# Kernel tuning notes

Measured on AMD Instinct MI355X. Metric: run time of the kernel, lower is better.

The kernel has to match this reference:

```python
import jax, jax.numpy as jnp
import numpy as np

DICT = 32768
TOP_K = 128
LN_EPS = 1e-5


def setup_inputs() -> dict:
    key = jax.random.key(0)
    k_x, k_we, k_be, k_wd, k_bd = jax.random.split(key, 5)
    B, S, D = 4, 2048, 768
    x = jax.random.normal(k_x, (B, S, D), dtype=jnp.float32)
    # nn.Linear stores weight as [out, in]; init scaled roughly like orthogonal gains
    W_enc = jax.random.normal(k_we, (DICT, D), dtype=jnp.float32) / np.sqrt(D)
    b_enc = jax.random.normal(k_be, (DICT,), dtype=jnp.float32) * 0.01
    W_dec = jax.random.normal(k_wd, (D, DICT), dtype=jnp.float32) * (0.1 / np.sqrt(DICT))
    b_dec = jax.random.normal(k_bd, (D,), dtype=jnp.float32) * 0.01
    ln_gamma = jnp.ones((DICT,), dtype=jnp.float32)
    ln_beta = jnp.zeros((DICT,), dtype=jnp.float32)
    return {"x": x, "W_enc": W_enc, "b_enc": b_enc, "ln_gamma": ln_gamma,
            "ln_beta": ln_beta, "W_dec": W_dec, "b_dec": b_dec}


def _layernorm(z, gamma, beta):
    mu = jnp.mean(z, axis=-1, keepdims=True)
    var = jnp.mean(jnp.square(z - mu), axis=-1, keepdims=True)
    return (z - mu) * jax.lax.rsqrt(var + LN_EPS) * gamma + beta


def _top_k_activation(z, k):
    # keep top-k values per row, zero elsewhere (scatter, like torch.scatter_)
    vals, idx = jax.lax.top_k(z, k)            # [B,S,k]
    out = jnp.zeros_like(z)
    return jnp.put_along_axis(out, idx, vals, axis=-1, inplace=False)


def reference(x, W_enc, b_enc, ln_gamma, ln_beta, W_dec, b_dec):
    # encoder: [B,S,D] @ [D,DICT] -> [B,S,DICT]
    z = jnp.einsum("bsd,fd->bsf", x, W_enc) + b_enc
    z = _layernorm(z, ln_gamma, ln_beta)
    z = jax.nn.relu(z)
    features = _top_k_activation(z, TOP_K)      # [B,S,DICT], mostly zero
    output = jnp.einsum("bsf,df->bsd", features, W_dec) + b_dec  # [B,S,D]
    return (output, features)
```

## Files before the change

kernel.cpp:

```cpp
#include <hip/hip_runtime.h>
#include <hip/hip_bf16.h>

#define R_TOT  8192
#define DIM    768
#define FDICT  32768
#define TOPK   128
#define LN_EPS 1e-5f
#define BAND_M 0.12f
#define BAND_CAP 192

using f32x4  = __attribute__((ext_vector_type(4))) float;
using short8 = __attribute__((ext_vector_type(8))) short;

__device__ inline short f2bf(float f) {
    __hip_bfloat16 h = __float2bfloat16(f);
    return *reinterpret_cast<short*>(&h);
}
__device__ inline float bf2f(short s) {
    return __uint_as_float(((unsigned)(unsigned short)s) << 16);
}
__device__ inline void load_lds16(const void* g, void* l) {
    __builtin_amdgcn_global_load_lds(
        (const __attribute__((address_space(1))) unsigned int*)g,
        (__attribute__((address_space(3))) unsigned int*)l, 16, 0, 0);
}

__global__ __launch_bounds__(256) void conv_bf16(
    const float* __restrict__ in, unsigned short* __restrict__ out, int n8)
{
    const int i0 = blockIdx.x * 256 + threadIdx.x;
    const int stride = gridDim.x * 256;
    for (int g = i0; g < n8; g += stride) {
        const float4 a = ((const float4*)in)[g * 2];
        const float4 b = ((const float4*)in)[g * 2 + 1];
        short8 v;
        v[0] = f2bf(a.x); v[1] = f2bf(a.y); v[2] = f2bf(a.z); v[3] = f2bf(a.w);
        v[4] = f2bf(b.x); v[5] = f2bf(b.y); v[6] = f2bf(b.z); v[7] = f2bf(b.w);
        ((short8*)out)[g] = v;
    }
}

__global__ __launch_bounds__(256) void enc_gemm(
    const unsigned short* __restrict__ Xb, const unsigned short* __restrict__ Wb,
    const float* __restrict__ benc, unsigned short* __restrict__ Zb)
{
    __shared__ __align__(16) unsigned short S[32768];

    const int t = threadIdx.x;
    const int w = t >> 6, l = t & 63;

    const int cpx = gridDim.x >> 3;
    const int swz = (blockIdx.x & 7) * cpx + (blockIdx.x >> 3);
    const long bm = (long)(swz >> 8) * 128;
    const long bn = (long)(swz & 255) * 128;

    const int wm = w >> 1, wn = w & 1;

    const unsigned short* ga = Xb + (bm + w * 32 + (l >> 3)) * DIM + (l & 7) * 8;
    const unsigned short* gb = Wb + (bn + w * 32 + (l >> 3)) * DIM + (l & 7) * 8;
    const int stg = w * 2048;

    f32x4 acc[4][4];
#pragma unroll
    for (int m = 0; m < 4; ++m)
#pragma unroll
        for (int n = 0; n < 4; ++n) acc[m][n] = (f32x4){0.f, 0.f, 0.f, 0.f};

    const int lrow = l & 15, lk = (l >> 4) * 8;

#pragma unroll
    for (int i = 0; i < 4; ++i) {
        load_lds16(ga + (size_t)i * 8 * DIM, S + stg + i * 512);
        load_lds16(gb + (size_t)i * 8 * DIM, S + 8192 + stg + i * 512);
    }
    ga += 64; gb += 64;
    __syncthreads();

#pragma unroll 1
    for (int kt = 0; kt < DIM / 64 - 1; ++kt) {
        const int nbo = ((kt & 1) ^ 1) * 16384;
        const int cbo = (kt & 1) * 16384;
#pragma unroll
        for (int i = 0; i < 4; ++i) {
            load_lds16(ga + (size_t)i * 8 * DIM, S + nbo + stg + i * 512);
            load_lds16(gb + (size_t)i * 8 * DIM, S + nbo + 8192 + stg + i * 512);
        }
        ga += 64; gb += 64;
        const unsigned short* rA = S + cbo;
        const unsigned short* rB = S + cbo + 8192;
#pragma unroll
        for (int ks = 0; ks < 2; ++ks) {
            short8 af[4], bfr[4];
#pragma unroll
            for (int m = 0; m < 4; ++m)
                af[m] = *(const short8*)&rA[(wm * 64 + m * 16 + lrow) * 64 + ks * 32 + lk];
#pragma unroll
            for (int n = 0; n < 4; ++n)
                bfr[n] = *(const short8*)&rB[(wn * 64 + n * 16 + lrow) * 64 + ks * 32 + lk];
#pragma unroll
            for (int m = 0; m < 4; ++m)
#pragma unroll
                for (int n = 0; n < 4; ++n)
                    acc[m][n] = __builtin_amdgcn_mfma_f32_16x16x32_bf16(
                        af[m], bfr[n], acc[m][n], 0, 0, 0);
        }
        __syncthreads();
    }

    {
        const int cbo = ((DIM / 64 - 1) & 1) * 16384;
        const unsigned short* rA = S + cbo;
        const unsigned short* rB = S + cbo + 8192;
#pragma unroll
        for (int ks = 0; ks < 2; ++ks) {
            short8 af[4], bfr[4];
#pragma unroll
            for (int m = 0; m < 4; ++m)
                af[m] = *(const short8*)&rA[(wm * 64 + m * 16 + lrow) * 64 + ks * 32 + lk];
#pragma unroll
            for (int n = 0; n < 4; ++n)
                bfr[n] = *(const short8*)&rB[(wn * 64 + n * 16 + lrow) * 64 + ks * 32 + lk];
#pragma unroll
            for (int m = 0; m < 4; ++m)
#pragma unroll
                for (int n = 0; n < 4; ++n)
                    acc[m][n] = __builtin_amdgcn_mfma_f32_16x16x32_bf16(
                        af[m], bfr[n], acc[m][n], 0, 0, 0);
        }
    }

    const int lr = l >> 4, lc = l & 15;
    float bias[4];
#pragma unroll
    for (int n = 0; n < 4; ++n) bias[n] = benc[bn + wn * 64 + n * 16 + lc];

    unsigned short* Cs = S;
#pragma unroll
    for (int m = 0; m < 4; ++m)
#pragma unroll
        for (int n = 0; n < 4; ++n)
#pragma unroll
            for (int q = 0; q < 4; ++q)
                Cs[(wm * 64 + m * 16 + lr * 4 + q) * 128 + wn * 64 + n * 16 + lc] =
                    (unsigned short)f2bf(acc[m][n][q] + bias[n]);
    __syncthreads();
#pragma unroll
    for (int i = 0; i < 8; ++i) {
        const int gidx = t + i * 256;
        const int row = gidx >> 4;
        const int c8  = (gidx & 15) * 8;
        const short8 v = *(const short8*)&Cs[row * 128 + c8];
        __builtin_nontemporal_store(v, (short8*)&Zb[(bm + row) * FDICT + bn + c8]);
    }
}

__global__ __launch_bounds__(1024) void topk_select(
    const unsigned short* __restrict__ Zb, const float* __restrict__ gamma,
    const float* __restrict__ beta, int* __restrict__ sel_idx,
    float* __restrict__ sel_val, int* __restrict__ band_idx,
    int* __restrict__ cdef, int* __restrict__ nband,
    float* __restrict__ muarr, float* __restrict__ sinvarr)
{
    __shared__ float    redf[32];
    __shared__ int      redi[16];
    __shared__ float    sf[3];
    __shared__ int      stot;
    __shared__ unsigned scomp[2];

    const int t = threadIdx.x;
    const int w = t >> 6;
    const long r = blockIdx.x;

    unsigned u[32];
    float sum = 0.f, sumsq = 0.f;
    const short8* Z8 = (const short8*)(Zb + r * (size_t)FDICT);
#pragma unroll
    for (int q = 0; q < 4; ++q) {
        const short8 v = Z8[q * 1024 + t];
#pragma unroll
        for (int j = 0; j < 8; ++j) {
            const float f = bf2f(v[j]);
            u[q * 8 + j] = __float_as_uint(f);
            sum += f; sumsq += f * f;
        }
    }
#pragma unroll
    for (int o = 32; o > 0; o >>= 1) {
        sum   += __shfl_down(sum, o, 64);
        sumsq += __shfl_down(sumsq, o, 64);
    }
    if ((t & 63) == 0) { redf[w] = sum; redf[16 + w] = sumsq; }
    __syncthreads();
    if (t == 0) {
        float s = 0.f, sq = 0.f;
        for (int i = 0; i < 16; ++i) { s += redf[i]; sq += redf[16 + i]; }
        const float mu = s / (float)FDICT;
        float var = sq / (float)FDICT - mu * mu;
        if (var < 0.f) var = 0.f;
        sf[0] = mu; sf[1] = 1.f / sqrtf(var + LN_EPS);
        scomp[0] = 0; scomp[1] = 0;
    }
    __syncthreads();
    const float mu = sf[0], sinv = sf[1];

    float vmax = 0.f;
#pragma unroll
    for (int q = 0; q < 4; ++q) {
        const size_t base = (size_t)(q * 1024 + t) * 8;
        const float4 g0 = *(const float4*)(gamma + base);
        const float4 g1 = *(const float4*)(gamma + base + 4);
        const float4 b0 = *(const float4*)(beta + base);
        const float4 b1 = *(const float4*)(beta + base + 4);
        const float gs[8] = {g0.x, g0.y, g0.z, g0.w, g1.x, g1.y, g1.z, g1.w};
        const float bs[8] = {b0.x, b0.y, b0.z, b0.w, b1.x, b1.y, b1.z, b1.w};
#pragma unroll
        for (int j = 0; j < 8; ++j) {
            const int i = q * 8 + j;
            const float a = fmaxf(
                fmaf((__uint_as_float(u[i]) - mu) * sinv, gs[j], bs[j]), 0.f);
            u[i] = __float_as_uint(a);
            vmax = fmaxf(vmax, a);
        }
    }
#pragma unroll
    for (int o = 32; o > 0; o >>= 1) vmax = fmaxf(vmax, __shfl_down(vmax, o, 64));
    if ((t & 63) == 0) redf[w] = vmax;
    __syncthreads();
    if (t == 0) {
        float m = 0.f;
        for (int i = 0; i < 16; ++i) m = fmaxf(m, redf[i]);
        sf[2] = m;
    }
    __syncthreads();

    float lo = 0.f, hi = sf[2] + 1e-6f;
#pragma unroll 1
    for (int it = 0; it < 9; ++it) {
        const float thr = 0.5f * (lo + hi);
        int cnt = 0;
#pragma unroll
        for (int i = 0; i < 32; ++i) cnt += (__uint_as_float(u[i]) > thr);
#pragma unroll
        for (int o = 32; o > 0; o >>= 1) cnt += __shfl_down(cnt, o, 64);
        if ((t & 63) == 0) redi[w] = cnt;
        __syncthreads();
        if (t == 0) {
            int s = 0;
            for (int i = 0; i < 16; ++i) s += redi[i];
            stot = s;
        }
        __syncthreads();
        if (stot >= TOPK) lo = thr; else hi = thr;
    }
    const float Tf = 0.5f * (lo + hi);
    const float thi = Tf + BAND_M, tlo = Tf - BAND_M;

#pragma unroll
    for (int i = 0; i < 32; ++i) {
        const float a = __uint_as_float(u[i]);
        const int idx = ((i >> 3) * 1024 + t) * 8 + (i & 7);
        if (a > thi) {
            const unsigned s = atomicAdd(&scomp[0], 1u);
            sel_idx[r * TOPK + s] = idx;
            sel_val[r * TOPK + s] = a;
        } else if (a >= tlo) {
            const unsigned s = atomicAdd(&scomp[1], 1u);
            if (s < BAND_CAP) band_idx[r * BAND_CAP + s] = idx;
        }
    }
    __syncthreads();
    if (t == 0) {
        cdef[r]  = (int)scomp[0];
        int nb = (int)scomp[1]; if (nb > BAND_CAP) nb = BAND_CAP;
        nband[r] = nb;
        muarr[r] = mu; sinvarr[r] = sinv;
    }
}

__global__ __launch_bounds__(256) void refine_select(
    const float* __restrict__ X, const float* __restrict__ Wenc,
    const float* __restrict__ benc, const float* __restrict__ gamma,
    const float* __restrict__ beta, const int* __restrict__ band_idx,
    const int* __restrict__ cdef, const int* __restrict__ nband,
    const float* __restrict__ muarr, const float* __restrict__ sinvarr,
    int* __restrict__ sel_idx, float* __restrict__ sel_val)
{
    __shared__ float xs[DIM];
    __shared__ float cval[BAND_CAP];
    __shared__ int   cidx[BAND_CAP];
    __shared__ int   scnt;
    const int t = threadIdx.x;
    const long r = blockIdx.x;
    const int w = t >> 6, l = t & 63;

    for (int i = t; i < DIM; i += 256) xs[i] = X[r * DIM + i];
    if (t == 0) scnt = 0;
    const int nb = nband[r];
    const int cd = cdef[r];
    int need = TOPK - cd; if (need > nb) need = nb;
    const double mu = (double)muarr[r], sinv = (double)sinvarr[r];
    __syncthreads();

    for (int c = w; c < nb; c += 4) {
        const int fi = band_idx[r * BAND_CAP + c];
        const float* wr = Wenc + (size_t)fi * DIM;
        double s = 0.0;
        for (int k = l; k < DIM; k += 64) s = fma((double)xs[k], (double)wr[k], s);
#pragma unroll
        for (int o = 32; o > 0; o >>= 1) s += __shfl_down(s, o, 64);
        if (l == 0) {
            const double z = s + (double)benc[fi];
            const double a = (z - mu) * sinv * (double)gamma[fi] + (double)beta[fi];
            cval[c] = fmaxf((float)a, 0.f);
            cidx[c] = fi;
        }
    }
    __syncthreads();
    if (t < nb) {
        const float v = cval[t];
        const int id = cidx[t];
        int rank = 0;
        for (int j = 0; j < nb; ++j) {
            const float vj = cval[j];
            rank += (vj > v) || (vj == v && cidx[j] < id);
        }
        if (rank < need) {
            const int s = atomicAdd(&scnt, 1);
            sel_idx[r * TOPK + cd + s] = id;
            sel_val[r * TOPK + cd + s] = v;
        }
    }
}

__global__ __launch_bounds__(256) void transposeWd(
    const float* __restrict__ Wd, unsigned short* __restrict__ WdTb)
{
    __shared__ float tile[32][33];
    const int fx = blockIdx.x * 32;
    const int dy = blockIdx.y * 32;
    const int tx = threadIdx.x & 31;
    const int ty = threadIdx.x >> 5;
    for (int i = ty; i < 32; i += 8)
        tile[i][tx] = Wd[(size_t)(dy + i) * FDICT + fx + tx];
    __syncthreads();
    for (int i = ty; i < 32; i += 8)
        WdTb[(size_t)(fx + i) * DIM + dy + tx] = (unsigned short)f2bf(tile[tx][i]);
}

__global__ __launch_bounds__(384) void decode(
    const int* __restrict__ sel_idx, const float* __restrict__ sel_val,
    const unsigned short* __restrict__ WdTb, const float* __restrict__ bdec,
    float* __restrict__ out)
{
    __shared__ int   sidx[TOPK];
    __shared__ float sval[TOPK];
    const int t = threadIdx.x;
    const long r = blockIdx.x;
    if (t < TOPK) { sidx[t] = sel_idx[r * TOPK + t]; sval[t] = sel_val[r * TOPK + t]; }
    __syncthreads();
    const float2 b2 = *(const float2*)(bdec + t * 2);
    float a0 = b2.x, a1 = b2.y;
    for (int j = 0; j < TOPK; ++j) {
        const unsigned wp = *(const unsigned*)(WdTb + (size_t)sidx[j] * DIM + t * 2);
        const float v = sval[j];
        a0 = fmaf(v, __uint_as_float((wp & 0xFFFFu) << 16), a0);
        a1 = fmaf(v, __uint_as_float(wp & 0xFFFF0000u), a1);
    }
    float2 o2; o2.x = a0; o2.y = a1;
    *(float2*)(out + r * DIM + t * 2) = o2;
}

__global__ __launch_bounds__(1024) void featfill(
    const int* __restrict__ sel_idx, const float* __restrict__ sel_val,
    float* __restrict__ feat)
{
    const int t = threadIdx.x;
    const long r = blockIdx.x;
    const f32x4 z4 = (f32x4){0.f, 0.f, 0.f, 0.f};
    f32x4* row4 = (f32x4*)(feat + r * FDICT);
    for (int i = t; i < FDICT / 4; i += 1024)
        __builtin_nontemporal_store(z4, &row4[i]);
    __syncthreads();
    if (t < TOPK)
        feat[r * FDICT + sel_idx[r * TOPK + t]] = sel_val[r * TOPK + t];
}

extern "C" void kernel_launch(void* const* d_in, const int* in_sizes, int n_in,
                              void* d_out, int out_size, void* d_ws, size_t ws_size,
                              hipStream_t stream)
{
    const float* x     = (const float*)d_in[0];
    const float* Wenc  = (const float*)d_in[1];
    const float* benc  = (const float*)d_in[2];
    const float* gamma = (const float*)d_in[3];
    const float* beta  = (const float*)d_in[4];
    const float* Wdec  = (const float*)d_in[5];
    const float* bdec  = (const float*)d_in[6];

    float* out  = (float*)d_out;
    float* feat = out + (size_t)R_TOT * DIM;

    unsigned short* Xb   = (unsigned short*)out;
    unsigned short* Zb   = (unsigned short*)feat;
    unsigned short* Wb   = (unsigned short*)((char*)feat + 536870912ull);
    unsigned short* WdTb = (unsigned short*)((char*)feat + 587202560ull);

    char* ws = (char*)d_ws;
    int*   sidx  = (int*)ws;
    float* sval  = (float*)(ws + (size_t)R_TOT * TOPK * 4);
    int*   bidx  = (int*)(ws + (size_t)R_TOT * TOPK * 8);
    int*   cdef  = (int*)(ws + (size_t)R_TOT * (TOPK * 8 + BAND_CAP * 4));
    int*   nbnd  = cdef + R_TOT;
    float* muarr = (float*)(nbnd + R_TOT);
    float* sinva = muarr + R_TOT;

    conv_bf16<<<1536, 256, 0, stream>>>(x,    Xb, R_TOT * DIM / 8);
    conv_bf16<<<2048, 256, 0, stream>>>(Wenc, Wb, FDICT * DIM / 8);
    enc_gemm<<<16384, 256, 0, stream>>>(Xb, Wb, benc, Zb);
    topk_select<<<R_TOT, 1024, 0, stream>>>(Zb, gamma, beta, sidx, sval,
                                            bidx, cdef, nbnd, muarr, sinva);
    refine_select<<<R_TOT, 256, 0, stream>>>(x, Wenc, benc, gamma, beta,
                                             bidx, cdef, nbnd, muarr, sinva,
                                             sidx, sval);
    transposeWd<<<dim3(FDICT / 32, DIM / 32), 256, 0, stream>>>(Wdec, WdTb);
    decode<<<R_TOT, 384, 0, stream>>>(sidx, sval, WdTb, bdec, out);
    featfill<<<R_TOT, 1024, 0, stream>>>(sidx, sval, feat);
}
```

Baseline: 2.190 ms.

## Rewrite encoder GEMM with 256x256 tiles, swizzled LDS and interleaved pipeline

The encoder GEMM now uses 256x256 output tiles per 512-thread block instead of 128x128 per 256-thread block, so each loaded element is reused more and global/LDS traffic per flop drops. LDS layout is XOR-swizzled to avoid bank conflicts. Loads for A and B of the next k-tile are split across phases of the compute loop, with explicit vmcnt waits, barriers and setprio around the MFMA bursts, to overlap memory with compute. It doubles LDS use to 128KB and raises register pressure (32 accumulators per wave), which risks lower occupancy and spills.

```diff
diff --git a/kernel.cpp b/kernel.cpp
--- a/kernel.cpp
+++ b/kernel.cpp
@@ -40,116 +40,155 @@
     }
 }
 
-__global__ __launch_bounds__(256) void enc_gemm(
+#define READ_A(P)                                                              \
+    af00 = *(const short8*)&Sb[abase + (2*(P))*1024 + sw0];                    \
+    af01 = *(const short8*)&Sb[abase + (2*(P))*1024 + sw1];                    \
+    af10 = *(const short8*)&Sb[abase + (2*(P)+1)*1024 + sw0];                  \
+    af11 = *(const short8*)&Sb[abase + (2*(P)+1)*1024 + sw1];
+
+#define DO_MFMA(P)                                                             \
+    __builtin_amdgcn_s_setprio(1);                                             \
+    _Pragma("unroll")                                                          \
+    for (int n = 0; n < 4; ++n) {                                              \
+        acc[2*(P)][n]   = __builtin_amdgcn_mfma_f32_16x16x32_bf16(af00, bf0[n], acc[2*(P)][n],   0,0,0); \
+        acc[2*(P)][n]   = __builtin_amdgcn_mfma_f32_16x16x32_bf16(af01, bf1[n], acc[2*(P)][n],   0,0,0); \
+        acc[2*(P)+1][n] = __builtin_amdgcn_mfma_f32_16x16x32_bf16(af10, bf0[n], acc[2*(P)+1][n], 0,0,0); \
+        acc[2*(P)+1][n] = __builtin_amdgcn_mfma_f32_16x16x32_bf16(af11, bf1[n], acc[2*(P)+1][n], 0,0,0); \
+    }                                                                          \
+    __builtin_amdgcn_s_setprio(0);
+
+__global__ __launch_bounds__(512, 2) void enc_gemm(
     const unsigned short* __restrict__ Xb, const unsigned short* __restrict__ Wb,
     const float* __restrict__ benc, unsigned short* __restrict__ Zb)
 {
-    __shared__ __align__(16) unsigned short S[32768];
+    __shared__ __align__(16) unsigned short S[65536];
 
     const int t = threadIdx.x;
     const int w = t >> 6, l = t & 63;
 
-    const int cpx = gridDim.x >> 3;
-    const int swz = (blockIdx.x & 7) * cpx + (blockIdx.x >> 3);
-    const long bm = (long)(swz >> 8) * 128;
-    const long bn = (long)(swz & 255) * 128;
-
-    const int wm = w >> 1, wn = w & 1;
-
-    const unsigned short* ga = Xb + (bm + w * 32 + (l >> 3)) * DIM + (l & 7) * 8;
-    const unsigned short* gb = Wb + (bn + w * 32 + (l >> 3)) * DIM + (l & 7) * 8;
-    const int stg = w * 2048;
-
-    f32x4 acc[4][4];
-#pragma unroll
-    for (int m = 0; m < 4; ++m)
+    const int cpx = (int)gridDim.x >> 3;
+    const int swz = ((int)blockIdx.x & 7) * cpx + ((int)blockIdx.x >> 3);
+    const long bm = (long)(swz >> 7) * 256;
+    const long bn = (long)(swz & 127) * 256;
+
+    const int wm = w >> 2, wn = w & 3;
+    const int lrow = l & 15, l4 = l >> 4;
+
+    const int sw0 = ((l4     ) ^ (lrow & 7)) * 8;
+    const int sw1 = ((4 + l4 ) ^ (lrow & 7)) * 8;
+    const int abase = wm * 8192 + lrow * 64;
+    const int bbase = 16384 + wn * 4096 + lrow * 64;
+
+    const int rh0 = w * 16 + (l >> 3);
+    const int rh1 = rh0 + 8;
+    const int gsl = ((l & 7) ^ (l >> 3)) * 8;
+    const unsigned short* pA00 = Xb + (bm +       rh0) * DIM + gsl;
+    const unsigned short* pA01 = Xb + (bm +       rh1) * DIM + gsl;
+    const unsigned short* pA10 = Xb + (bm + 128 + rh0) * DIM + gsl;
+    const unsigned short* pA11 = Xb + (bm + 128 + rh1) * DIM + gsl;
+    const unsigned short* pB00 = Wb + (bn +       rh0) * DIM + gsl;
+    const unsigned short* pB01 = Wb + (bn +       rh1) * DIM + gsl;
+    const unsigned short* pB10 = Wb + (bn + 128 + rh0) * DIM + gsl;
+    const unsigned short* pB11 = Wb + (bn + 128 + rh1) * DIM + gsl;
+    const int d00 = w * 1024;
+    const int d01 = w * 1024 + 512;
+
+    f32x4 acc[8][4];
+#pragma unroll
+    for (int m = 0; m < 8; ++m)
 #pragma unroll
         for (int n = 0; n < 4; ++n) acc[m][n] = (f32x4){0.f, 0.f, 0.f, 0.f};
 
-    const int lrow = l & 15, lk = (l >> 4) * 8;
-
-#pragma unroll
-    for (int i = 0; i < 4; ++i) {
-        load_lds16(ga + (size_t)i * 8 * DIM, S + stg + i * 512);
-        load_lds16(gb + (size_t)i * 8 * DIM, S + 8192 + stg + i * 512);
-    }
-    ga += 64; gb += 64;
-    __syncthreads();
+    load_lds16(pA00, S + d00);
+    load_lds16(pA01, S + d01);
+    load_lds16(pA10, S + 8192 + d00);
+    load_lds16(pA11, S + 8192 + d01);
+    load_lds16(pB00, S + 16384 + d00);
+    load_lds16(pB01, S + 16384 + d01);
+    load_lds16(pB10, S + 16384 + 8192 + d00);
+    load_lds16(pB11, S + 16384 + 8192 + d01);
+    pA00 += 64; pA01 += 64; pA10 += 64; pA11 += 64;
+    pB00 += 64; pB01 += 64; pB10 += 64; pB11 += 64;
+
+    short8 bf0[4], bf1[4];
+    short8 af00, af01, af10, af11;
 
 #pragma unroll 1
-    for (int kt = 0; kt < DIM / 64 - 1; ++kt) {
-        const int nbo = ((kt & 1) ^ 1) * 16384;
-        const int cbo = (kt & 1) * 16384;
-#pragma unroll
-        for (int i = 0; i < 4; ++i) {
-            load_lds16(ga + (size_t)i * 8 * DIM, S + nbo + stg + i * 512);
-            load_lds16(gb + (size_t)i * 8 * DIM, S + nbo + 8192 + stg + i * 512);
-        }
-        ga += 64; gb += 64;
-        const unsigned short* rA = S + cbo;
-        const unsigned short* rB = S + cbo + 8192;
-#pragma unroll
-        for (int ks = 0; ks < 2; ++ks) {
-            short8 af[4], bfr[4];
-#pragma unroll
-            for (int m = 0; m < 4; ++m)
-                af[m] = *(const short8*)&rA[(wm * 64 + m * 16 + lrow) * 64 + ks * 32 + lk];
-#pragma unroll
-            for (int n = 0; n < 4; ++n)
-                bfr[n] = *(const short8*)&rB[(wn * 64 + n * 16 + lrow) * 64 + ks * 32 + lk];
-#pragma unroll
-            for (int m = 0; m < 4; ++m)
-#pragma unroll
-                for (int n = 0; n < 4; ++n)
-                    acc[m][n] = __builtin_amdgcn_mfma_f32_16x16x32_bf16(
-                        af[m], bfr[n], acc[m][n], 0, 0, 0);
-        }
-        __syncthreads();
-    }
-
-    {
-        const int cbo = ((DIM / 64 - 1) & 1) * 16384;
-        const unsigned short* rA = S + cbo;
-        const unsigned short* rB = S + cbo + 8192;
-#pragma unroll
-        for (int ks = 0; ks < 2; ++ks) {
-            short8 af[4], bfr[4];
-#pragma unroll
-            for (int m = 0; m < 4; ++m)
-                af[m] = *(const short8*)&rA[(wm * 64 + m * 16 + lrow) * 64 + ks * 32 + lk];
-#pragma unroll
-            for (int n = 0; n < 4; ++n)
-                bfr[n] = *(const short8*)&rB[(wn * 64 + n * 16 + lrow) * 64 + ks * 32 + lk];
-#pragma unroll
-            for (int m = 0; m < 4; ++m)
-#pragma unroll
-                for (int n = 0; n < 4; ++n)
-                    acc[m][n] = __builtin_amdgcn_mfma_f32_16x16x32_bf16(
-                        af[m], bfr[n], acc[m][n], 0, 0, 0);
-        }
-    }
-
-    const int lr = l >> 4, lc = l & 15;
+    for (int kt = 0; kt < 12; ++kt) {
+        const unsigned short* Sb = S + (kt & 1) * 32768;
+        unsigned short*       Sn = S + ((kt & 1) ^ 1) * 32768;
+
+        if (kt < 11) {
+            load_lds16(pA00, Sn + d00);
+            load_lds16(pA01, Sn + d01);
+            load_lds16(pA10, Sn + 8192 + d00);
+            load_lds16(pA11, Sn + 8192 + d01);
+            asm volatile("s_waitcnt vmcnt(4)" ::: "memory");
+        } else {
+            asm volatile("s_waitcnt vmcnt(0)" ::: "memory");
+        }
+        __builtin_amdgcn_s_barrier();
+#pragma unroll
+        for (int n = 0; n < 4; ++n) {
+            bf0[n] = *(const short8*)&Sb[bbase + n * 1024 + sw0];
+            bf1[n] = *(const short8*)&Sb[bbase + n * 1024 + sw1];
+        }
+        READ_A(0)
+        DO_MFMA(0)
+        asm volatile("" ::: "memory");
+        __builtin_amdgcn_s_barrier();
+
+        READ_A(1)
+        if (kt < 11) {
+            load_lds16(pB00, Sn + 16384 + d00);
+            load_lds16(pB01, Sn + 16384 + d01);
+            load_lds16(pB10, Sn + 16384 + 8192 + d00);
+            load_lds16(pB11, Sn + 16384 + 8192 + d01);
+        }
+        asm volatile("" ::: "memory");
+        __builtin_amdgcn_s_barrier();
+        DO_MFMA(1)
+        asm volatile("" ::: "memory");
+        __builtin_amdgcn_s_barrier();
+
+        READ_A(2)
+        asm volatile("" ::: "memory");
+        __builtin_amdgcn_s_barrier();
+        DO_MFMA(2)
+        asm volatile("" ::: "memory");
+        __builtin_amdgcn_s_barrier();
+
+        READ_A(3)
+        asm volatile("" ::: "memory");
+        __builtin_amdgcn_s_barrier();
+        DO_MFMA(3)
+        asm volatile("" ::: "memory");
+        __builtin_amdgcn_s_barrier();
+
+        pA00 += 64; pA01 += 64; pA10 += 64; pA11 += 64;
+        pB00 += 64; pB01 += 64; pB10 += 64; pB11 += 64;
+    }
+
+    __syncthreads();
     float bias[4];
 #pragma unroll
-    for (int n = 0; n < 4; ++n) bias[n] = benc[bn + wn * 64 + n * 16 + lc];
-
+    for (int n = 0; n < 4; ++n) bias[n] = benc[bn + wn * 64 + n * 16 + lrow];
     unsigned short* Cs = S;
 #pragma unroll
-    for (int m = 0; m < 4; ++m)
+    for (int m = 0; m < 8; ++m)
 #pragma unroll
         for (int n = 0; n < 4; ++n)
 #pragma unroll
             for (int q = 0; q < 4; ++q)
-                Cs[(wm * 64 + m * 16 + lr * 4 + q) * 128 + wn * 64 + n * 16 + lc] =
+                Cs[(wm * 128 + m * 16 + l4 * 4 + q) * 256 + wn * 64 + n * 16 + lrow] =
                     (unsigned short)f2bf(acc[m][n][q] + bias[n]);
     __syncthreads();
 #pragma unroll
-    for (int i = 0; i < 8; ++i) {
-        const int gidx = t + i * 256;
-        const int row = gidx >> 4;
-        const int c8  = (gidx & 15) * 8;
-        const short8 v = *(const short8*)&Cs[row * 128 + c8];
+    for (int it = 0; it < 16; ++it) {
+        const int g = t + it * 512;
+        const int row = g >> 5;
+        const int c8 = (g & 31) * 8;
+        const short8 v = *(const short8*)&Cs[row * 256 + c8];
         __builtin_nontemporal_store(v, (short8*)&Zb[(bm + row) * FDICT + bn + c8]);
     }
 }
@@ -416,7 +455,7 @@
 
     conv_bf16<<<1536, 256, 0, stream>>>(x,    Xb, R_TOT * DIM / 8);
     conv_bf16<<<2048, 256, 0, stream>>>(Wenc, Wb, FDICT * DIM / 8);
-    enc_gemm<<<16384, 256, 0, stream>>>(Xb, Wb, benc, Zb);
+    enc_gemm<<<4096, 512, 0, stream>>>(Xb, Wb, benc, Zb);
     topk_select<<<R_TOT, 1024, 0, stream>>>(Zb, gamma, beta, sidx, sval,
                                             bidx, cdef, nbnd, muarr, sinva);
     refine_select<<<R_TOT, 256, 0, stream>>>(x, Wenc, benc, gamma, beta,
```

Result: faster. 2.041 ms (-6.8%).
